# Optimization experiments

Hardware: AMD Instinct MI355X
Metric: run time of the kernel (lower is better)

Reference implementation:

```python
import jax, jax.numpy as jnp
import numpy as np


def setup_inputs() -> dict:
    key = jax.random.key(0)
    n_samples, n_points, dims = 16, 2048, 64
    h = jax.random.normal(key, (n_samples, n_points, dims), dtype=jnp.float32)
    return {"h": h, "K": 16}


def reference(h, K):
    """Pairwise squared distance + K nearest neighbors -> edge list.

    h : (n_samples, n_points, dims)
    Returns (knn_dist, dst, src):
      knn_dist : (n_samples, n_points, K) squared distances to the K nearest points
      dst, src : (n_samples*n_points*K,) int32 globally-offset edge endpoints
    """
    n_samples, n_points, _ = h.shape
    # d[b, i, j] = ||h[b,i]||^2 + ||h[b,j]||^2 - 2 <h[b,i], h[b,j]>
    x2s = jnp.sum(h * h, axis=-1, keepdims=True)          # (s, n, 1)
    d = x2s + jnp.swapaxes(x2s, -1, -2) - 2.0 * jnp.einsum('bnd,bmd->bnm', h, h)
    # smallest-K == top-K of negated distances (matches torch.topk largest=False order)
    neg_vals, k_indices = jax.lax.top_k(-d, K)            # (s, n, K)
    knn_dist = -neg_vals
    # edge list with per-sample node-id offsets (matches the torch flattening)
    src = jnp.broadcast_to(jnp.arange(n_points, dtype=k_indices.dtype)[None, :, None],
                           k_indices.shape)
    offset = (jnp.arange(n_samples, dtype=k_indices.dtype) * n_points)[:, None, None]
    dst = (k_indices + offset).reshape(-1)
    src = (src + offset).reshape(-1)
    return knn_dist, dst, src
```

## Files before the change

kernel.cpp:

```cpp
#include <hip/hip_runtime.h>
#include <hip/hip_fp16.h>
#include <cfloat>


typedef _Float16 half8 __attribute__((ext_vector_type(8)));
typedef float    f32x4 __attribute__((ext_vector_type(4)));

constexpr int NS = 16, NP = 2048, ND = 64, KK = 16;
constexpr int NWV = 4;
constexpr int NT  = NWV * 64;
constexpr int RB  = 32;
constexpr int ITN = RB / 16;
constexpr int JW  = NP / NWV;
constexpr int NJT = JW / 16;
constexpr int MS  = 17;
constexpr int RCAP = 128;
constexpr int RSTR = RCAP + 1;
constexpr float MARGIN = 1.0f;

__global__ void prep_kernel(const float* __restrict__ h, float* __restrict__ x2,
                            _Float16* __restrict__ hh)
{
    int g = blockIdx.x * 256 + threadIdx.x;
    const float4* row = (const float4*)(h + (size_t)g * ND);
    int ph = g & 15;
    float a0 = 0.f, a1 = 0.f, a2 = 0.f, a3 = 0.f;
    #pragma unroll
    for (int k = 0; k < 16; ++k) {
        float4 v = row[(k + ph) & 15];
        a0 = fmaf(v.x, v.x, a0); a1 = fmaf(v.y, v.y, a1);
        a2 = fmaf(v.z, v.z, a2); a3 = fmaf(v.w, v.w, a3);
    }
    x2[g] = (a0 + a1) + (a2 + a3);
    _Float16* dst = hh + (size_t)g * ND;
    #pragma unroll
    for (int k = 0; k < 8; ++k) {
        float4 v0 = row[2 * k], v1 = row[2 * k + 1];
        half8 p;
        p[0] = (_Float16)v0.x; p[1] = (_Float16)v0.y;
        p[2] = (_Float16)v0.z; p[3] = (_Float16)v0.w;
        p[4] = (_Float16)v1.x; p[5] = (_Float16)v1.y;
        p[6] = (_Float16)v1.z; p[7] = (_Float16)v1.w;
        *(half8*)(dst + k * 8) = p;
    }
}

__device__ __forceinline__ bool lexlt(float a, int ja, float b, int jb)
{
    return (a < b) || (a == b && ja < jb);
}
__device__ __forceinline__ void insert16x(float (&d)[KK], int (&ix)[KK],
                                          float v, int j)
{
    #pragma unroll
    for (int p = KK - 1; p > 0; --p) {
        bool sh = lexlt(v, j, d[p - 1], ix[p - 1]);
        bool he = lexlt(v, j, d[p], ix[p]);
        float nd = sh ? d[p - 1] : (he ? v : d[p]);
        int   ni = sh ? ix[p - 1] : (he ? j : ix[p]);
        d[p] = nd; ix[p] = ni;
    }
    if (lexlt(v, j, d[0], ix[0])) { d[0] = v; ix[0] = j; }
}

__global__ __launch_bounds__(NT, 4)
void knn_mfma(const float* __restrict__ h, const _Float16* __restrict__ hh,
              const float* __restrict__ x2g, float* __restrict__ out)
{
    __shared__ __align__(16) float smem[8544];
    float* ldsx2  = smem;
    float* mw     = smem + 2048;
    float* ldsthr = smem + 2176;
    int*   rcnt   = (int*)(smem + 2208);
    int*   ring   = (int*)(smem + 2240);
    float* md     = smem + 6368;
    int*   mi     = (int*)(smem + 7456);

    const int t   = threadIdx.x;
    const int ln  = t & 63;
    const int qd  = ln >> 4;
    const int cl  = ln & 15;
    const int q   = t >> 6;
    const int row = ln & 31;
    const int jh  = ln >> 5;
    const int s   = blockIdx.x >> 6;
    const int rb  = blockIdx.x & 63;
    const int rowbase = rb * RB;
    const float*    __restrict__ hs  = h  + (size_t)s * NP * ND;
    const _Float16* __restrict__ hhs = hh + (size_t)s * NP * ND;

    ((float4*)ldsx2)[t]       = ((const float4*)(x2g + s * NP))[t];
    ((float4*)ldsx2)[t + 256] = ((const float4*)(x2g + s * NP))[t + 256];
    if (t < RB) rcnt[t] = 0;

    half8 ifr[ITN][2];
    #pragma unroll
    for (int it = 0; it < ITN; ++it) {
        const _Float16* ap = hhs + (size_t)(rowbase + it * 16 + cl) * ND + qd * 8;
        ifr[it][0] = *(const half8*)(ap);
        ifr[it][1] = *(const half8*)(ap + 32);
    }
    __syncthreads();

    const int jbase = q * JW;

    float t1[ITN], t2[ITN], t3[ITN], t4[ITN];
    #pragma unroll
    for (int it = 0; it < ITN; ++it)
        { t1[it] = FLT_MAX; t2[it] = FLT_MAX; t3[it] = FLT_MAX; t4[it] = FLT_MAX; }

    #pragma unroll 2
    for (int jt = 0; jt < NJT; ++jt) {
        const int j0 = jbase + jt * 16;
        const _Float16* bp = hhs + (size_t)(j0 + cl) * ND + qd * 8;
        half8 jlo = *(const half8*)(bp);
        half8 jhi = *(const half8*)(bp + 32);
        f32x4 x2q = *(const f32x4*)(ldsx2 + j0 + qd * 4);

        #pragma unroll
        for (int it = 0; it < ITN; ++it) {
            f32x4 acc;
            acc = __builtin_amdgcn_mfma_f32_16x16x32_f16(
                      jlo, ifr[it][0], (f32x4){0.f, 0.f, 0.f, 0.f}, 0, 0, 0);
            acc = __builtin_amdgcn_mfma_f32_16x16x32_f16(
                      jhi, ifr[it][1], acc, 0, 0, 0);
            #pragma unroll
            for (int r = 0; r < 4; ++r) {
                float v  = fmaf(-2.f, acc[r], x2q[r]);
                float n1 = fminf(t1[it], v);
                float n2 = __builtin_amdgcn_fmed3f(t1[it], t2[it], v);
                float n3 = __builtin_amdgcn_fmed3f(t2[it], t3[it], v);
                float n4 = __builtin_amdgcn_fmed3f(t3[it], t4[it], v);
                t1[it] = n1; t2[it] = n2; t3[it] = n3; t4[it] = n4;
            }
        }
    }

    #pragma unroll
    for (int it = 0; it < ITN; ++it) {
        #pragma unroll
        for (int lvl = 0; lvl < 2; ++lvl) {
            const int mask = 16 << lvl;
            float b1 = __shfl_xor(t1[it], mask), b2 = __shfl_xor(t2[it], mask);
            float b3 = __shfl_xor(t3[it], mask), b4 = __shfl_xor(t4[it], mask);
            float m1 = fminf(t1[it], b4), m2 = fminf(t2[it], b3);
            float m3 = fminf(t3[it], b2), m4 = fminf(t4[it], b1);
            float u1 = fminf(m1, m3), u3 = fmaxf(m1, m3);
            float u2 = fminf(m2, m4), u4 = fmaxf(m2, m4);
            t1[it] = fminf(u1, u2); t2[it] = fmaxf(u1, u2);
            t3[it] = fminf(u3, u4); t4[it] = fmaxf(u3, u4);
        }
    }
    if (qd == 0) {
        mw[q * 32 + cl]      = t4[0];
        mw[q * 32 + 16 + cl] = t4[1];
    }
    __syncthreads();
    if (q == 0 && ln < 32) {
        float m0 = mw[row], m1 = mw[32 + row];
        float m2 = mw[64 + row], m3 = mw[96 + row];
        ldsthr[row] = fmaxf(fmaxf(m0, m1), fmaxf(m2, m3)) + MARGIN;
    }
    __syncthreads();

    float thrv[ITN];
    #pragma unroll
    for (int it = 0; it < ITN; ++it) thrv[it] = ldsthr[it * 16 + cl];

    #pragma unroll 2
    for (int jt = 0; jt < NJT; ++jt) {
        const int j0 = jbase + jt * 16;
        const _Float16* bp = hhs + (size_t)(j0 + cl) * ND + qd * 8;
        half8 jlo = *(const half8*)(bp);
        half8 jhi = *(const half8*)(bp + 32);
        f32x4 x2q = *(const f32x4*)(ldsx2 + j0 + qd * 4);

        #pragma unroll
        for (int it = 0; it < ITN; ++it) {
            f32x4 acc;
            acc = __builtin_amdgcn_mfma_f32_16x16x32_f16(
                      jlo, ifr[it][0], (f32x4){0.f, 0.f, 0.f, 0.f}, 0, 0, 0);
            acc = __builtin_amdgcn_mfma_f32_16x16x32_f16(
                      jhi, ifr[it][1], acc, 0, 0, 0);
            #pragma unroll
            for (int r = 0; r < 4; ++r) {
                float d2 = fmaf(-2.f, acc[r], x2q[r]);
                if (d2 < thrv[it]) {
                    int rw = it * 16 + cl;
                    int slot = atomicAdd(&rcnt[rw], 1);
                    if (slot < RCAP) ring[rw * RSTR + slot] = j0 + qd * 4 + r;
                }
            }
        }
    }
    __syncthreads();

    const int myrow = rowbase + row;
    float4 A[16];
    {
        const float4* ra = (const float4*)(hs + (size_t)myrow * ND);
        #pragma unroll
        for (int k = 0; k < 16; ++k) A[k] = ra[k];
    }
    float x2i;
    {
        float a0 = 0.f, a1 = 0.f, a2 = 0.f, a3 = 0.f;
        #pragma unroll
        for (int k = 0; k < 16; ++k) {
            a0 = fmaf(A[k].x, A[k].x, a0); a1 = fmaf(A[k].y, A[k].y, a1);
            a2 = fmaf(A[k].z, A[k].z, a2); a3 = fmaf(A[k].w, A[k].w, a3);
        }
        x2i = (a0 + a1) + (a2 + a3);
    }
    float dist[KK]; int idx[KK];
    #pragma unroll
    for (int k = 0; k < KK; ++k) { dist[k] = FLT_MAX; idx[k] = 0; }

    const int cntR = min(rcnt[row], RCAP);
    const int w8 = q * 2 + jh;
    #pragma unroll 1
    for (int k = w8; k < cntR; k += 8) {
        int j = ring[row * RSTR + k];
        const float4* cv = (const float4*)(hs + (size_t)j * ND);
        float a0 = 0.f, a1 = 0.f, a2 = 0.f, a3 = 0.f;
        #pragma unroll
        for (int kk = 0; kk < 16; ++kk) {
            float4 c = cv[kk];
            a0 = fmaf(A[kk].x, c.x, a0); a1 = fmaf(A[kk].y, c.y, a1);
            a2 = fmaf(A[kk].z, c.z, a2); a3 = fmaf(A[kk].w, c.w, a3);
        }
        float dotv = (a0 + a1) + (a2 + a3);
        float d2 = fmaf(-2.0f, dotv, x2i + ldsx2[j]);
        if (lexlt(d2, j, dist[KK - 1], idx[KK - 1]))
            insert16x(dist, idx, d2, j);
    }

    #pragma unroll 1
    for (int k = 0; k < KK; ++k) {
        float v  = __shfl(dist[k], row + 32);
        int   jv = __shfl(idx[k],  row + 32);
        bool need = (ln < 32) && lexlt(v, jv, dist[KK - 1], idx[KK - 1]);
        if (!__any(need)) break;
        if (need) insert16x(dist, idx, v, jv);
    }
    __syncthreads();
    #pragma unroll 1
    for (int lvl = 0; lvl < 2; ++lvl) {
        const int step = 1 << lvl;
        const int m    = (step << 1) - 1;
        const bool pub = ((q & m) == step) && ln < 32;
        const int reg  = q >> (lvl + 1);
        if (pub) {
            #pragma unroll
            for (int k = 0; k < KK; ++k) {
                md[(reg * RB + row) * MS + k] = dist[k];
                mi[(reg * RB + row) * MS + k] = idx[k];
            }
        }
        __syncthreads();
        if ((q & m) == 0) {
            #pragma unroll 1
            for (int k = 0; k < KK; ++k) {
                float v  = md[(reg * RB + row) * MS + k];
                int   jv = mi[(reg * RB + row) * MS + k];
                bool need = (ln < 32) && lexlt(v, jv, dist[KK - 1], idx[KK - 1]);
                if (!__any(need)) break;
                if (need) insert16x(dist, idx, v, jv);
            }
        }
        __syncthreads();
    }

    if (q == 0 && ln < 32) {
        const int off = s * NP;
        const size_t rg = (size_t)off + myrow;
        float* o0 = out + rg * KK;
        float* o1 = out + (size_t)NS * NP * KK + rg * KK;
        float* o2 = out + (size_t)2 * NS * NP * KK + rg * KK;
        #pragma unroll
        for (int k = 0; k < KK; ++k) o0[k] = dist[k];
        #pragma unroll
        for (int k = 0; k < KK; ++k) o1[k] = (float)(idx[k] + off);
        #pragma unroll
        for (int k = 0; k < KK; ++k) o2[k] = (float)(off + myrow);
    }
}

extern "C" void kernel_launch(void* const* d_in, const int* in_sizes, int n_in,
                              void* d_out, int out_size, void* d_ws, size_t ws_size,
                              hipStream_t stream)
{
    const float* h = (const float*)d_in[0];
    float* out = (float*)d_out;
    float*    x2 = (float*)d_ws;
    _Float16* hh = (_Float16*)(x2 + NS * NP);

    hipLaunchKernelGGL(prep_kernel, dim3(NS * NP / 256), dim3(256), 0, stream,
                       h, x2, hh);
    hipLaunchKernelGGL(knn_mfma, dim3(NS * (NP / RB)), dim3(NT), 0, stream,
                       h, hh, x2, out);
}
```

Before: 219.7 us.

## Software-prefetch j-tiles in both MFMA passes and remap blocks per XCD

Both distance passes now keep a four-deep register ring of upcoming j-tile fragments and x2 values, loading tile t+4 while tile t is fed to the MFMAs. This is meant to hide global load latency behind the matrix and selection work. Block indices are also remapped so that all blocks belonging to one sample land on the same XCD, which should improve L2 reuse of that sample's fp16 data. The cost is higher register pressure, which may reduce occupancy.

```diff
diff --git a/kernel.cpp b/kernel.cpp
--- a/kernel.cpp
+++ b/kernel.cpp
@@ -13,6 +13,7 @@
 constexpr int ITN = RB / 16;
 constexpr int JW  = NP / NWV;
 constexpr int NJT = JW / 16;
+constexpr int PF  = 4;
 constexpr int MS  = 17;
 constexpr int RCAP = 128;
 constexpr int RSTR = RCAP + 1;
@@ -83,8 +84,11 @@
     const int q   = t >> 6;
     const int row = ln & 31;
     const int jh  = ln >> 5;
-    const int s   = blockIdx.x >> 6;
-    const int rb  = blockIdx.x & 63;
+    const int bid = blockIdx.x;
+    const int xcd = bid & 7;
+    const int kb  = bid >> 3;
+    const int s   = xcd + ((kb & 1) << 3);
+    const int rb  = kb >> 1;
     const int rowbase = rb * RB;
     const float*    __restrict__ hs  = h  + (size_t)s * NP * ND;
     const _Float16* __restrict__ hhs = hh + (size_t)s * NP * ND;
@@ -103,35 +107,48 @@
     __syncthreads();
 
     const int jbase = q * JW;
+    const _Float16* __restrict__ jrow0 = hhs + (size_t)(jbase + cl) * ND + qd * 8;
+
+    auto loadj = [&](int jt, half8 &lo, half8 &hi, f32x4 &xq) {
+        const _Float16* bp = jrow0 + (size_t)jt * (16 * ND);
+        lo = *(const half8*)(bp);
+        hi = *(const half8*)(bp + 32);
+        xq = *(const f32x4*)(ldsx2 + jbase + jt * 16 + qd * 4);
+    };
 
     float t1[ITN], t2[ITN], t3[ITN], t4[ITN];
     #pragma unroll
     for (int it = 0; it < ITN; ++it)
         { t1[it] = FLT_MAX; t2[it] = FLT_MAX; t3[it] = FLT_MAX; t4[it] = FLT_MAX; }
 
-    #pragma unroll 2
-    for (int jt = 0; jt < NJT; ++jt) {
-        const int j0 = jbase + jt * 16;
-        const _Float16* bp = hhs + (size_t)(j0 + cl) * ND + qd * 8;
-        half8 jlo = *(const half8*)(bp);
-        half8 jhi = *(const half8*)(bp + 32);
-        f32x4 x2q = *(const f32x4*)(ldsx2 + j0 + qd * 4);
-
-        #pragma unroll
-        for (int it = 0; it < ITN; ++it) {
-            f32x4 acc;
-            acc = __builtin_amdgcn_mfma_f32_16x16x32_f16(
-                      jlo, ifr[it][0], (f32x4){0.f, 0.f, 0.f, 0.f}, 0, 0, 0);
-            acc = __builtin_amdgcn_mfma_f32_16x16x32_f16(
-                      jhi, ifr[it][1], acc, 0, 0, 0);
+    {
+        half8 plo[PF], phi[PF]; f32x4 pxq[PF];
+        #pragma unroll
+        for (int p = 0; p < PF; ++p) loadj(p, plo[p], phi[p], pxq[p]);
+
+        for (int t0 = 0; t0 < NJT; t0 += PF) {
             #pragma unroll
-            for (int r = 0; r < 4; ++r) {
-                float v  = fmaf(-2.f, acc[r], x2q[r]);
-                float n1 = fminf(t1[it], v);
-                float n2 = __builtin_amdgcn_fmed3f(t1[it], t2[it], v);
-                float n3 = __builtin_amdgcn_fmed3f(t2[it], t3[it], v);
-                float n4 = __builtin_amdgcn_fmed3f(t3[it], t4[it], v);
-                t1[it] = n1; t2[it] = n2; t3[it] = n3; t4[it] = n4;
+            for (int p = 0; p < PF; ++p) {
+                half8 clo = plo[p], chi = phi[p]; f32x4 cxq = pxq[p];
+                int nx = t0 + p + PF;
+                if (nx < NJT) loadj(nx, plo[p], phi[p], pxq[p]);
+                #pragma unroll
+                for (int it = 0; it < ITN; ++it) {
+                    f32x4 acc;
+                    acc = __builtin_amdgcn_mfma_f32_16x16x32_f16(
+                              clo, ifr[it][0], (f32x4){0.f, 0.f, 0.f, 0.f}, 0, 0, 0);
+                    acc = __builtin_amdgcn_mfma_f32_16x16x32_f16(
+                              chi, ifr[it][1], acc, 0, 0, 0);
+                    #pragma unroll
+                    for (int r = 0; r < 4; ++r) {
+                        float v  = fmaf(-2.f, acc[r], cxq[r]);
+                        float n1 = fminf(t1[it], v);
+                        float n2 = __builtin_amdgcn_fmed3f(t1[it], t2[it], v);
+                        float n3 = __builtin_amdgcn_fmed3f(t2[it], t3[it], v);
+                        float n4 = __builtin_amdgcn_fmed3f(t3[it], t4[it], v);
+                        t1[it] = n1; t2[it] = n2; t3[it] = n3; t4[it] = n4;
+                    }
+                }
             }
         }
     }
@@ -167,28 +184,34 @@
     #pragma unroll
     for (int it = 0; it < ITN; ++it) thrv[it] = ldsthr[it * 16 + cl];
 
-    #pragma unroll 2
-    for (int jt = 0; jt < NJT; ++jt) {
-        const int j0 = jbase + jt * 16;
-        const _Float16* bp = hhs + (size_t)(j0 + cl) * ND + qd * 8;
-        half8 jlo = *(const half8*)(bp);
-        half8 jhi = *(const half8*)(bp + 32);
-        f32x4 x2q = *(const f32x4*)(ldsx2 + j0 + qd * 4);
-
-        #pragma unroll
-        for (int it = 0; it < ITN; ++it) {
-            f32x4 acc;
-            acc = __builtin_amdgcn_mfma_f32_16x16x32_f16(
-                      jlo, ifr[it][0], (f32x4){0.f, 0.f, 0.f, 0.f}, 0, 0, 0);
-            acc = __builtin_amdgcn_mfma_f32_16x16x32_f16(
-                      jhi, ifr[it][1], acc, 0, 0, 0);
+    {
+        half8 plo[PF], phi[PF]; f32x4 pxq[PF];
+        #pragma unroll
+        for (int p = 0; p < PF; ++p) loadj(p, plo[p], phi[p], pxq[p]);
+
+        for (int t0 = 0; t0 < NJT; t0 += PF) {
             #pragma unroll
-            for (int r = 0; r < 4; ++r) {
-                float d2 = fmaf(-2.f, acc[r], x2q[r]);
-                if (d2 < thrv[it]) {
-                    int rw = it * 16 + cl;
-                    int slot = atomicAdd(&rcnt[rw], 1);
-                    if (slot < RCAP) ring[rw * RSTR + slot] = j0 + qd * 4 + r;
+            for (int p = 0; p < PF; ++p) {
+                half8 clo = plo[p], chi = phi[p]; f32x4 cxq = pxq[p];
+                const int j0 = jbase + (t0 + p) * 16;
+                int nx = t0 + p + PF;
+                if (nx < NJT) loadj(nx, plo[p], phi[p], pxq[p]);
+                #pragma unroll
+                for (int it = 0; it < ITN; ++it) {
+                    f32x4 acc;
+                    acc = __builtin_amdgcn_mfma_f32_16x16x32_f16(
+                              clo, ifr[it][0], (f32x4){0.f, 0.f, 0.f, 0.f}, 0, 0, 0);
+                    acc = __builtin_amdgcn_mfma_f32_16x16x32_f16(
+                              chi, ifr[it][1], acc, 0, 0, 0);
+                    #pragma unroll
+                    for (int r = 0; r < 4; ++r) {
+                        float d2 = fmaf(-2.f, acc[r], cxq[r]);
+                        if (d2 < thrv[it]) {
+                            int rw = it * 16 + cl;
+                            int slot = atomicAdd(&rcnt[rw], 1);
+                            if (slot < RCAP) ring[rw * RSTR + slot] = j0 + qd * 4 + r;
+                        }
+                    }
                 }
             }
         }
```

After: 215.8 us. No clear change (-1.8%).

## Fuse prep kernel into KNN kernel and remap blocks by XCD

Applied to the files above, without the earlier changes.

Removes the separate prep kernel that wrote fp16 copies and squared norms to workspace. Each block now recomputes all 2048 row norms of its sample into LDS and converts fp32 rows to fp16 on the fly inside both MFMA passes. Block IDs are remapped so each XCD serves two fixed samples, which should improve L2 locality. The trade is a launch and a workspace round trip removed in exchange for double-size fp32 global loads per tile, extra conversion instructions, and redundant norm computation in each of 64 blocks per sample.

```diff
diff --git a/kernel.cpp b/kernel.cpp
--- a/kernel.cpp
+++ b/kernel.cpp
@@ -18,33 +18,6 @@
 constexpr int RSTR = RCAP + 1;
 constexpr float MARGIN = 1.0f;
 
-__global__ void prep_kernel(const float* __restrict__ h, float* __restrict__ x2,
-                            _Float16* __restrict__ hh)
-{
-    int g = blockIdx.x * 256 + threadIdx.x;
-    const float4* row = (const float4*)(h + (size_t)g * ND);
-    int ph = g & 15;
-    float a0 = 0.f, a1 = 0.f, a2 = 0.f, a3 = 0.f;
-    #pragma unroll
-    for (int k = 0; k < 16; ++k) {
-        float4 v = row[(k + ph) & 15];
-        a0 = fmaf(v.x, v.x, a0); a1 = fmaf(v.y, v.y, a1);
-        a2 = fmaf(v.z, v.z, a2); a3 = fmaf(v.w, v.w, a3);
-    }
-    x2[g] = (a0 + a1) + (a2 + a3);
-    _Float16* dst = hh + (size_t)g * ND;
-    #pragma unroll
-    for (int k = 0; k < 8; ++k) {
-        float4 v0 = row[2 * k], v1 = row[2 * k + 1];
-        half8 p;
-        p[0] = (_Float16)v0.x; p[1] = (_Float16)v0.y;
-        p[2] = (_Float16)v0.z; p[3] = (_Float16)v0.w;
-        p[4] = (_Float16)v1.x; p[5] = (_Float16)v1.y;
-        p[6] = (_Float16)v1.z; p[7] = (_Float16)v1.w;
-        *(half8*)(dst + k * 8) = p;
-    }
-}
-
 __device__ __forceinline__ bool lexlt(float a, int ja, float b, int jb)
 {
     return (a < b) || (a == b && ja < jb);
@@ -63,9 +36,18 @@
     if (lexlt(v, j, d[0], ix[0])) { d[0] = v; ix[0] = j; }
 }
 
+__device__ __forceinline__ half8 cvt8(float4 a, float4 b)
+{
+    half8 p;
+    p[0] = (_Float16)a.x; p[1] = (_Float16)a.y;
+    p[2] = (_Float16)a.z; p[3] = (_Float16)a.w;
+    p[4] = (_Float16)b.x; p[5] = (_Float16)b.y;
+    p[6] = (_Float16)b.z; p[7] = (_Float16)b.w;
+    return p;
+}
+
 __global__ __launch_bounds__(NT, 4)
-void knn_mfma(const float* __restrict__ h, const _Float16* __restrict__ hh,
-              const float* __restrict__ x2g, float* __restrict__ out)
+void knn_fused(const float* __restrict__ h, float* __restrict__ out)
 {
     __shared__ __align__(16) float smem[8544];
     float* ldsx2  = smem;
@@ -83,26 +65,42 @@
     const int q   = t >> 6;
     const int row = ln & 31;
     const int jh  = ln >> 5;
-    const int s   = blockIdx.x >> 6;
-    const int rb  = blockIdx.x & 63;
+    const int bid = blockIdx.x;
+    const int xcd = bid & 7;
+    const int kb  = bid >> 3;
+    const int s   = xcd + ((kb & 1) << 3);
+    const int rb  = kb >> 1;
     const int rowbase = rb * RB;
-    const float*    __restrict__ hs  = h  + (size_t)s * NP * ND;
-    const _Float16* __restrict__ hhs = hh + (size_t)s * NP * ND;
-
-    ((float4*)ldsx2)[t]       = ((const float4*)(x2g + s * NP))[t];
-    ((float4*)ldsx2)[t + 256] = ((const float4*)(x2g + s * NP))[t + 256];
+    const float* __restrict__ hs = h + (size_t)s * NP * ND;
+
     if (t < RB) rcnt[t] = 0;
 
+    #pragma unroll 1
+    for (int u = 0; u < 8; ++u) {
+        const int r = t * 8 + u;
+        const float4* rowp = (const float4*)(hs + (size_t)r * ND);
+        const int ph = r & 15;
+        float a0 = 0.f, a1 = 0.f, a2 = 0.f, a3 = 0.f;
+        #pragma unroll
+        for (int k = 0; k < 16; ++k) {
+            float4 v = rowp[(k + ph) & 15];
+            a0 = fmaf(v.x, v.x, a0); a1 = fmaf(v.y, v.y, a1);
+            a2 = fmaf(v.z, v.z, a2); a3 = fmaf(v.w, v.w, a3);
+        }
+        ldsx2[r] = (a0 + a1) + (a2 + a3);
+    }
+
     half8 ifr[ITN][2];
     #pragma unroll
     for (int it = 0; it < ITN; ++it) {
-        const _Float16* ap = hhs + (size_t)(rowbase + it * 16 + cl) * ND + qd * 8;
-        ifr[it][0] = *(const half8*)(ap);
-        ifr[it][1] = *(const half8*)(ap + 32);
+        const float* ap = hs + (size_t)(rowbase + it * 16 + cl) * ND + qd * 8;
+        ifr[it][0] = cvt8(*(const float4*)(ap),      *(const float4*)(ap + 4));
+        ifr[it][1] = cvt8(*(const float4*)(ap + 32), *(const float4*)(ap + 36));
     }
     __syncthreads();
 
     const int jbase = q * JW;
+    const float* __restrict__ jrow0 = hs + (size_t)(jbase + cl) * ND + qd * 8;
 
     float t1[ITN], t2[ITN], t3[ITN], t4[ITN];
     #pragma unroll
@@ -111,11 +109,14 @@
 
     #pragma unroll 2
     for (int jt = 0; jt < NJT; ++jt) {
-        const int j0 = jbase + jt * 16;
-        const _Float16* bp = hhs + (size_t)(j0 + cl) * ND + qd * 8;
-        half8 jlo = *(const half8*)(bp);
-        half8 jhi = *(const half8*)(bp + 32);
-        f32x4 x2q = *(const f32x4*)(ldsx2 + j0 + qd * 4);
+        const float* bp = jrow0 + (size_t)jt * (16 * ND);
+        float4 va = *(const float4*)(bp);
+        float4 vb = *(const float4*)(bp + 4);
+        float4 vc = *(const float4*)(bp + 32);
+        float4 vd = *(const float4*)(bp + 36);
+        f32x4 xq = *(const f32x4*)(ldsx2 + jbase + jt * 16 + qd * 4);
+        half8 jlo = cvt8(va, vb);
+        half8 jhi = cvt8(vc, vd);
 
         #pragma unroll
         for (int it = 0; it < ITN; ++it) {
@@ -126,7 +127,7 @@
                       jhi, ifr[it][1], acc, 0, 0, 0);
             #pragma unroll
             for (int r = 0; r < 4; ++r) {
-                float v  = fmaf(-2.f, acc[r], x2q[r]);
+                float v  = fmaf(-2.f, acc[r], xq[r]);
                 float n1 = fminf(t1[it], v);
                 float n2 = __builtin_amdgcn_fmed3f(t1[it], t2[it], v);
                 float n3 = __builtin_amdgcn_fmed3f(t2[it], t3[it], v);
@@ -169,11 +170,15 @@
 
     #pragma unroll 2
     for (int jt = 0; jt < NJT; ++jt) {
+        const float* bp = jrow0 + (size_t)jt * (16 * ND);
+        float4 va = *(const float4*)(bp);
+        float4 vb = *(const float4*)(bp + 4);
+        float4 vc = *(const float4*)(bp + 32);
+        float4 vd = *(const float4*)(bp + 36);
+        f32x4 xq = *(const f32x4*)(ldsx2 + jbase + jt * 16 + qd * 4);
+        half8 jlo = cvt8(va, vb);
+        half8 jhi = cvt8(vc, vd);
         const int j0 = jbase + jt * 16;
-        const _Float16* bp = hhs + (size_t)(j0 + cl) * ND + qd * 8;
-        half8 jlo = *(const half8*)(bp);
-        half8 jhi = *(const half8*)(bp + 32);
-        f32x4 x2q = *(const f32x4*)(ldsx2 + j0 + qd * 4);
 
         #pragma unroll
         for (int it = 0; it < ITN; ++it) {
@@ -184,7 +189,7 @@
                       jhi, ifr[it][1], acc, 0, 0, 0);
             #pragma unroll
             for (int r = 0; r < 4; ++r) {
-                float d2 = fmaf(-2.f, acc[r], x2q[r]);
+                float d2 = fmaf(-2.f, acc[r], xq[r]);
                 if (d2 < thrv[it]) {
                     int rw = it * 16 + cl;
                     int slot = atomicAdd(&rcnt[rw], 1);
@@ -292,11 +297,6 @@
 {
     const float* h = (const float*)d_in[0];
     float* out = (float*)d_out;
-    float*    x2 = (float*)d_ws;
-    _Float16* hh = (_Float16*)(x2 + NS * NP);
-
-    hipLaunchKernelGGL(prep_kernel, dim3(NS * NP / 256), dim3(256), 0, stream,
-                       h, x2, hh);
-    hipLaunchKernelGGL(knn_mfma, dim3(NS * (NP / RB)), dim3(NT), 0, stream,
-                       h, hh, x2, out);
-}
+    hipLaunchKernelGGL(knn_fused, dim3(NS * (NP / RB)), dim3(NT), 0, stream,
+                       h, out);
+}
```

Result: slower. 333.7 us (+51.9%).
